# Performance work log

Measured on AMD Instinct MI355X. Metric: run time of the kernel, lower is better.

## Reference

```python
import jax, jax.numpy as jnp
import numpy as np
from jax import lax

B, IMG = 2, 512
FMC, HID, A, NC = 1024, 512, 9, 21
RED, POOL, TOP, IOU_THR = 16, 7, 20, 0.3
NEG = -1e30
# 3 scales x 3 aspect ratios (w, h)
ANCHOR_WH = np.array([[s * np.sqrt(r), s / np.sqrt(r)] for s in (64.0, 128.0, 256.0) for r in (0.5, 1.0, 2.0)], dtype=np.float32)


def conv(x, w, b, stride, pad):
    y = lax.conv_general_dilated(x, w, (stride, stride), pad, dimension_numbers=('NCHW', 'OIHW', 'NCHW'))
    return y + b[None, :, None, None]


def make_anchors(H, W, stride):
    cy = (jnp.arange(H, dtype=jnp.float32) + 0.5) * stride
    cx = (jnp.arange(W, dtype=jnp.float32) + 0.5) * stride
    cyg, cxg = jnp.meshgrid(cy, cx, indexing='ij')  # [H,W]
    wh = jnp.asarray(ANCHOR_WH)  # [A,2]
    w2 = wh[None, None, :, 0] / 2
    h2 = wh[None, None, :, 1] / 2
    cxg = cxg[:, :, None]
    cyg = cyg[:, :, None]
    boxes = jnp.stack([cxg - w2, cyg - h2, cxg + w2, cyg + h2], axis=-1)  # [H,W,A,4]
    return boxes.reshape(-1, 4)


def box_iou(b, boxes):
    # b [4], boxes [N,4], (x1,y1,x2,y2)
    ix1 = jnp.maximum(b[0], boxes[:, 0])
    iy1 = jnp.maximum(b[1], boxes[:, 1])
    ix2 = jnp.minimum(b[2], boxes[:, 2])
    iy2 = jnp.minimum(b[3], boxes[:, 3])
    inter = jnp.maximum(ix2 - ix1, 0.0) * jnp.maximum(iy2 - iy1, 0.0)
    ab = jnp.maximum(b[2] - b[0], 0.0) * jnp.maximum(b[3] - b[1], 0.0)
    ar = jnp.maximum(boxes[:, 2] - boxes[:, 0], 0.0) * jnp.maximum(boxes[:, 3] - boxes[:, 1], 0.0)
    return inter / (ab + ar - inter + 1e-8)


def nms_one(boxes, scores):
    # greedy NMS, fixed TOP selections
    n = scores.shape[0]
    idxs = jnp.arange(n)

    def step(s, _):
        i = jnp.argmax(s)
        b, sc = boxes[i], s[i]
        s = jnp.where((box_iou(b, boxes) > IOU_THR) | (idxs == i), NEG, s)
        return s, (b, sc)

    _, (bs, ss) = lax.scan(step, scores, None, length=TOP)
    return bs, ss  # [TOP,4], [TOP]


def roi_align_one(fm_b, boxes):
    # fm_b [C,H,W], boxes [R,4] in image coords -> [R,C,POOL,POOL]
    C, H, W = fm_b.shape
    b = boxes / RED
    t = (jnp.arange(POOL, dtype=jnp.float32) + 0.5) / POOL
    xs = b[:, 0:1] + jnp.maximum(b[:, 2] - b[:, 0], 0.0)[:, None] * t[None]  # [R,P]
    ys = b[:, 1:2] + jnp.maximum(b[:, 3] - b[:, 1], 0.0)[:, None] * t[None]
    x = jnp.clip(xs[:, None, :], 0.0, W - 1.0) * jnp.ones((1, POOL, 1), jnp.float32)  # [R,P,P]
    y = jnp.clip(ys[:, :, None], 0.0, H - 1.0) * jnp.ones((1, 1, POOL), jnp.float32)
    x0f, y0f = jnp.floor(x), jnp.floor(y)
    x0, y0 = x0f.astype(jnp.int32), y0f.astype(jnp.int32)
    x1 = jnp.minimum(x0 + 1, W - 1)
    y1 = jnp.minimum(y0 + 1, H - 1)
    lx, ly = x - x0f, y - y0f
    v00 = fm_b[:, y0, x0]
    v01 = fm_b[:, y0, x1]
    v10 = fm_b[:, y1, x0]
    v11 = fm_b[:, y1, x1]  # [C,R,P,P]
    out = v00 * (1 - ly) * (1 - lx) + v01 * (1 - ly) * lx + v10 * ly * (1 - lx) + v11 * ly * lx
    return out.transpose(1, 0, 2, 3)


def setup_inputs() -> dict:
    key = jax.random.key(0)
    ks = jax.random.split(key, 16)
    s = 0.02
    return {
        'img': jax.random.normal(ks[0], (B, 3, IMG, IMG), jnp.float32),
        'img_id': jnp.arange(B, dtype=jnp.int32),
        'cnn_w': jax.random.normal(ks[1], (FMC, 3, RED, RED), jnp.float32) * s,
        'cnn_b': jnp.zeros((FMC,), jnp.float32),
        'rpn_w': jax.random.normal(ks[2], (HID, FMC, 3, 3), jnp.float32) * s,
        'rpn_b': jnp.zeros((HID,), jnp.float32),
        'rpn_reg_w': jax.random.normal(ks[3], (A * 4, HID, 1, 1), jnp.float32) * s,
        'rpn_reg_b': jnp.zeros((A * 4,), jnp.float32),
        'rpn_cls_w': jax.random.normal(ks[4], (A, HID, 1, 1), jnp.float32) * s,
        'rpn_cls_b': jnp.zeros((A,), jnp.float32),
        'fc_w': jax.random.normal(ks[5], (FMC * POOL * POOL, 1024), jnp.float32) * 0.005,
        'fc_b': jnp.zeros((1024,), jnp.float32),
        'reg_w': jax.random.normal(ks[6], (1024, 4), jnp.float32) * s,
        'reg_b': jnp.zeros((4,), jnp.float32),
        'cls_w': jax.random.normal(ks[7], (1024, NC), jnp.float32) * s,
        'cls_b': jnp.zeros((NC,), jnp.float32),
    }


def reference(img, img_id, cnn_w, cnn_b, rpn_w, rpn_b, rpn_reg_w, rpn_reg_b, rpn_cls_w, rpn_cls_b, fc_w, fc_b, reg_w, reg_b, cls_w, cls_b):
    fm = jax.nn.relu(conv(img, cnn_w, cnn_b, RED, 'VALID'))  # [B,1024,32,32]
    Bn, C, H, W = fm.shape
    # sliding-window(3x3, stride 1) + per-slice RPN == 3x3 SAME conv + 1x1 heads
    h = jax.nn.relu(conv(fm, rpn_w, rpn_b, 1, 'SAME'))
    rpn_reg = conv(h, rpn_reg_w, rpn_reg_b, 1, 'SAME').transpose(0, 2, 3, 1).reshape(Bn, -1, 4)  # (h,w,a) order
    rpn_cls = conv(h, rpn_cls_w, rpn_cls_b, 1, 'SAME').transpose(0, 2, 3, 1).reshape(Bn, -1)
    anchors = make_anchors(H, W, RED)  # [H*W*A,4]
    nms_reg, nms_cls = jax.vmap(nms_one)(rpn_reg + anchors[None], rpn_cls)  # [B,TOP,4],[B,TOP]
    pooled = jax.vmap(roi_align_one)(fm[img_id], nms_reg)  # [B,TOP,C,P,P]
    flat = pooled.reshape(Bn * TOP, -1)
    hf = jax.nn.relu(flat @ fc_w + fc_b)
    rcnn_reg = (hf @ reg_w + reg_b).reshape(Bn, -1, 4)
    rcnn_cls = (hf @ cls_w + cls_b).reshape(Bn, TOP, -1)
    return rpn_reg, rpn_cls, nms_reg, nms_cls, rcnn_reg, rcnn_cls, anchors
```

## Files before the change

### kernel.cpp

```cpp
#include <hip/hip_runtime.h>
#include <math.h>


#define NEGV (-1e30f)

typedef unsigned short u16;
typedef float v4f __attribute__((ext_vector_type(4)));
typedef short short8 __attribute__((ext_vector_type(8)));

#define O_RPN_REG 0
#define O_RPN_CLS 73728
#define O_NMS_REG 92160
#define O_NMS_CLS 92320
#define O_RCNN_REG 92360
#define O_RCNN_CLS 92520
#define O_ANCH 93360

#define W_FM   0u
#define W_ZERO 2097152u
#define W_PROP 3145728u
#define W_SCR  3219456u
#define W_FLAT 3237888u
#define W_HF   5244928u
#define W_A1H  5285888u
#define W_A1L  6072320u
#define W_B1H  6858752u
#define W_B1L  7251968u
#define W_FMH  7645184u
#define W_FML  8693760u
#define W_B2H  9742336u
#define W_B2L  12101632u
#define W_PART 14460928u

static __device__ __forceinline__ float relu_(float v) { return fmaxf(v, 0.0f); }

static __device__ __forceinline__ void gload16(const void* g, void* l) {
    __builtin_amdgcn_global_load_lds(
        (const __attribute__((address_space(1))) unsigned int*)g,
        (__attribute__((address_space(3))) unsigned int*)l, 16, 0, 0);
}

static __device__ __forceinline__ u16 bf16_rtne(float x) {
    unsigned int u = __float_as_uint(x);
    unsigned int r = u + 0x7fffu + ((u >> 16) & 1u);
    return (u16)(r >> 16);
}
static __device__ __forceinline__ void split2(float x, u16& h, u16& l) {
    h = bf16_rtne(x);
    const float hf = __uint_as_float(((unsigned int)h) << 16);
    l = bf16_rtne(x - hf);
}
static __device__ __forceinline__ void split8_store(const float* v, u16* dsth, u16* dstl) {
    uint4 H, Lo;
    u16 h0, l0, h1, l1;
    split2(v[0], h0, l0); split2(v[1], h1, l1);
    H.x = (unsigned)h0 | ((unsigned)h1 << 16); Lo.x = (unsigned)l0 | ((unsigned)l1 << 16);
    split2(v[2], h0, l0); split2(v[3], h1, l1);
    H.y = (unsigned)h0 | ((unsigned)h1 << 16); Lo.y = (unsigned)l0 | ((unsigned)l1 << 16);
    split2(v[4], h0, l0); split2(v[5], h1, l1);
    H.z = (unsigned)h0 | ((unsigned)h1 << 16); Lo.z = (unsigned)l0 | ((unsigned)l1 << 16);
    split2(v[6], h0, l0); split2(v[7], h1, l1);
    H.w = (unsigned)h0 | ((unsigned)h1 << 16); Lo.w = (unsigned)l0 | ((unsigned)l1 << 16);
    *(uint4*)dsth = H; *(uint4*)dstl = Lo;
}

static __device__ __forceinline__ void anchor_wh(int a, float& w2, float& h2) {
    double s = (a < 3) ? 64.0 : (a < 6) ? 128.0 : 256.0;
    int rm = a - (a / 3) * 3;
    double r = (rm == 0) ? 0.5 : (rm == 1) ? 1.0 : 2.0;
    double sq = sqrt(r);
    w2 = (float)(s * sq) * 0.5f;
    h2 = (float)(s / sq) * 0.5f;
}

__global__ __launch_bounds__(256) void k_prep_all(
        const float* __restrict__ img, u16* __restrict__ a1h, u16* __restrict__ a1l,
        float* __restrict__ zbuf,
        const float* __restrict__ cnnw, u16* __restrict__ b1h, u16* __restrict__ b1l,
        const float* __restrict__ rpnw, u16* __restrict__ b2h, u16* __restrict__ b2l) {
    __shared__ __align__(16) u16 sh[9216];
    __shared__ __align__(16) u16 sl[9216];
    const int bx = blockIdx.x, tid = threadIdx.x;
    if (bx < 1536) {
        if (bx == 0 && tid < 64) zbuf[tid] = 0.0f;
        const int idx = bx * 256 + tid;
        const int m = idx / 192, kq = (idx - m * 192) * 4;
        const int b = m >> 10, i = (m >> 5) & 31, j = m & 31;
        const int c = kq >> 8, rem = kq & 255, y = rem >> 4, x = rem & 15;
        const float4 v = *(const float4*)(img + ((size_t)((b * 3 + c) * 512 + i * 16 + y)) * 512 + j * 16 + x);
        ushort4 H, Lo;
        split2(v.x, H.x, Lo.x); split2(v.y, H.y, Lo.y);
        split2(v.z, H.z, Lo.z); split2(v.w, H.w, Lo.w);
        *(ushort4*)(a1h + (size_t)idx * 4) = H;
        *(ushort4*)(a1l + (size_t)idx * 4) = Lo;
    } else if (bx < 2304) {
        const int idx = (bx - 1536) * 256 + tid;
        const float4 v = *(const float4*)(cnnw + (size_t)idx * 4);
        ushort4 H, Lo;
        split2(v.x, H.x, Lo.x); split2(v.y, H.y, Lo.y);
        split2(v.z, H.z, Lo.z); split2(v.w, H.w, Lo.w);
        *(ushort4*)(b1h + (size_t)idx * 4) = H;
        *(ushort4*)(b1l + (size_t)idx * 4) = Lo;
    } else {
        const int oc = bx - 2304;
        const float* p = rpnw + (size_t)oc * 9216;
        for (int i = tid * 4; i < 9216; i += 1024) {
            const float4 v = *(const float4*)(p + i);
            ushort4 H, Lo;
            split2(v.x, H.x, Lo.x); split2(v.y, H.y, Lo.y);
            split2(v.z, H.z, Lo.z); split2(v.w, H.w, Lo.w);
            *(ushort4*)(sh + i) = H;
            *(ushort4*)(sl + i) = Lo;
        }
        __syncthreads();
        const int ic4 = tid * 4;
#pragma unroll
        for (int d = 0; d < 9; ++d) {
            ushort4 H, Lo;
            H.x = sh[(ic4 + 0) * 9 + d]; Lo.x = sl[(ic4 + 0) * 9 + d];
            H.y = sh[(ic4 + 1) * 9 + d]; Lo.y = sl[(ic4 + 1) * 9 + d];
            H.z = sh[(ic4 + 2) * 9 + d]; Lo.z = sl[(ic4 + 2) * 9 + d];
            H.w = sh[(ic4 + 3) * 9 + d]; Lo.w = sl[(ic4 + 3) * 9 + d];
            const size_t o = (size_t)oc * 9216 + d * 1024 + ic4;
            *(ushort4*)(b2h + o) = H;
            *(ushort4*)(b2l + o) = Lo;
        }
    }
}

template<int MODE>
__global__ __launch_bounds__(256, 3) void k_gemm(
        const u16* __restrict__ Agh, const u16* __restrict__ Agl,
        const u16* __restrict__ Bgh, const u16* __restrict__ Bgl,
        const float* __restrict__ bias, float* __restrict__ Cout, float* __restrict__ Cout2,
        const int KA, const int KB, const int nchunk, const int ldc, const int do_bias_relu,
        u16* __restrict__ outH, u16* __restrict__ outL, const float* __restrict__ zbuf) {
    __shared__ __align__(16) u16 AsH[2 * 128 * 32];
    __shared__ __align__(16) u16 AsL[2 * 128 * 32];
    __shared__ __align__(16) u16 BsH[2 * 64 * 32];
    __shared__ __align__(16) u16 BsL[2 * 64 * 32];
    const int tid = threadIdx.x;
    const int w = tid >> 6, L = tid & 63;
    const int q = L >> 4, lr = L & 15;
    const int wm = w >> 1, wn = w & 1;
    const int m0 = blockIdx.x * 128, n0 = blockIdx.y * 64;
    const int zbase = blockIdx.z * nchunk;
    float* C;
    if (MODE == 1) {
        C = (blockIdx.z < 4) ? (Cout + (size_t)blockIdx.z * (2048u * 512u))
                             : (Cout2 + (size_t)(blockIdx.z - 4) * (2048u * 512u));
    } else {
        C = (blockIdx.z == 0) ? Cout : Cout2;
    }
    const int seg = L & 3, rsub = L >> 2;

    u16* lseg[6];
    int lsz[6];
    const u16* gbase[6];
    int arow_b[6], arow_i[6], arow_j[6];
    int kindv[6];
#pragma unroll
    for (int s = 0; s < 6; ++s) {
        const int idx = w * 6 + s;
        int kind, inst;
        if (idx < 8)       { kind = 0; inst = idx; }
        else if (idx < 16) { kind = 1; inst = idx - 8; }
        else if (idx < 20) { kind = 2; inst = idx - 16; }
        else               { kind = 3; inst = idx - 20; }
        kindv[s] = kind;
        const int r = inst * 16 + rsub;
        u16* lb = (kind == 0) ? AsH : (kind == 1) ? AsL : (kind == 2) ? BsH : BsL;
        lseg[s] = lb + r * 32 + seg * 8;
        lsz[s] = (kind < 2) ? (128 * 32) : (64 * 32);
        arow_b[s] = 0; arow_i[s] = 0; arow_j[s] = 0;
        if (kind >= 2) {
            const u16* gb = (kind == 2) ? Bgh : Bgl;
            gbase[s] = gb + (size_t)(n0 + r) * KB + seg * 8;
        } else if (MODE == 0) {
            const u16* gb = (kind == 0) ? Agh : Agl;
            gbase[s] = gb + (size_t)(m0 + r) * KA + seg * 8;
        } else {
            const int m = m0 + r;
            arow_b[s] = m >> 10; arow_i[s] = (m >> 5) & 31; arow_j[s] = m & 31;
            gbase[s] = (kind == 0) ? Agh : Agl;
        }
    }

    v4f acc[4][2];
#pragma unroll
    for (int t = 0; t < 4; ++t)
#pragma unroll
        for (int u2 = 0; u2 < 2; ++u2) acc[t][u2] = (v4f){0.f, 0.f, 0.f, 0.f};

#define ISSUE(c_, bb_) do { \
    int d_, ic_, kB_; \
    if (MODE == 0) { const int g_ = zbase + (c_); kB_ = g_ * 32; d_ = 0; ic_ = kB_; } \
    else { const int g_ = zbase + (c_); d_ = g_ >> 5; ic_ = (g_ & 31) << 5; kB_ = d_ * 1024 + ic_; } \
    const int di_ = d_ / 3, dj_ = d_ - di_ * 3; \
    _Pragma("unroll") \
    for (int s = 0; s < 6; ++s) { \
        const u16* gsrc_; \
        if (kindv[s] >= 2) gsrc_ = gbase[s] + kB_; \
        else if (MODE == 0) gsrc_ = gbase[s] + ic_; \
        else { \
            const int y_ = arow_i[s] + di_ - 1, x_ = arow_j[s] + dj_ - 1; \
            const bool ok_ = ((unsigned)y_ < 32u) && ((unsigned)x_ < 32u); \
            const int yc_ = ok_ ? y_ : 0, xc_ = ok_ ? x_ : 0; \
            const u16* ga_ = gbase[s] + (size_t)((arow_b[s] * 32 + yc_) * 32 + xc_) * 1024 + ic_ + seg * 8; \
            gsrc_ = ok_ ? ga_ : (const u16*)zbuf; \
        } \
        gload16(gsrc_, lseg[s] + (bb_) * lsz[s]); \
    } \
} while (0)

    int cur = 0;
    ISSUE(0, 0);
    for (int c = 0; c < nchunk; ++c) {
        __syncthreads();
        if (c + 1 < nchunk) ISSUE(c + 1, cur ^ 1);
        const int ao = cur * (128 * 32), bo = cur * (64 * 32);
        short8 ah[4], al[4], bh[2], bl[2];
#pragma unroll
        for (int t = 0; t < 4; ++t) {
            ah[t] = *(const short8*)(AsH + ao + (wm * 64 + t * 16 + lr) * 32 + q * 8);
            al[t] = *(const short8*)(AsL + ao + (wm * 64 + t * 16 + lr) * 32 + q * 8);
        }
#pragma unroll
        for (int u2 = 0; u2 < 2; ++u2) {
            bh[u2] = *(const short8*)(BsH + bo + (wn * 32 + u2 * 16 + lr) * 32 + q * 8);
            bl[u2] = *(const short8*)(BsL + bo + (wn * 32 + u2 * 16 + lr) * 32 + q * 8);
        }
#pragma unroll
        for (int t = 0; t < 4; ++t)
#pragma unroll
            for (int u2 = 0; u2 < 2; ++u2) {
                acc[t][u2] = __builtin_amdgcn_mfma_f32_16x16x32_bf16(ah[t], bh[u2], acc[t][u2], 0, 0, 0);
                acc[t][u2] = __builtin_amdgcn_mfma_f32_16x16x32_bf16(ah[t], bl[u2], acc[t][u2], 0, 0, 0);
                acc[t][u2] = __builtin_amdgcn_mfma_f32_16x16x32_bf16(al[t], bh[u2], acc[t][u2], 0, 0, 0);
            }
        cur ^= 1;
    }
#undef ISSUE

#pragma unroll
    for (int t = 0; t < 4; ++t) {
        const int row = m0 + wm * 64 + t * 16 + q * 4;
#pragma unroll
        for (int u2 = 0; u2 < 2; ++u2) {
            const int col = n0 + wn * 32 + u2 * 16 + lr;
            const float bv = do_bias_relu ? bias[col] : 0.f;
#pragma unroll
            for (int r = 0; r < 4; ++r) {
                float vv = acc[t][u2][r];
                if (do_bias_relu) vv = relu_(vv + bv);
                C[(size_t)(row + r) * ldc + col] = vv;
                if (MODE == 0 && outH != nullptr) {
                    u16 hh, ll; split2(vv, hh, ll);
                    outH[(size_t)(row + r) * 1024 + col] = hh;
                    outL[(size_t)(row + r) * 1024 + col] = ll;
                }
            }
        }
    }
}

__global__ void k_c1_reduce(const float* __restrict__ p1, const float* __restrict__ cb,
                            float* __restrict__ fm, u16* __restrict__ fmh, u16* __restrict__ fml) {
    const size_t o = ((size_t)blockIdx.x * 256 + threadIdx.x) * 4;
    float4 a = *(const float4*)(fm + o);
    const float4 b4 = *(const float4*)(p1 + o);
    const float4 bb = *(const float4*)(cb + (o & 1023));
    a.x = relu_(a.x + b4.x + bb.x);
    a.y = relu_(a.y + b4.y + bb.y);
    a.z = relu_(a.z + b4.z + bb.z);
    a.w = relu_(a.w + b4.w + bb.w);
    *(float4*)(fm + o) = a;
    ushort4 H, Lo;
    split2(a.x, H.x, Lo.x); split2(a.y, H.y, Lo.y);
    split2(a.z, H.z, Lo.z); split2(a.w, H.w, Lo.w);
    *(ushort4*)(fmh + o) = H;
    *(ushort4*)(fml + o) = Lo;
}

__global__ __launch_bounds__(256) void k_rpn_heads2(const float* __restrict__ partA,
        const float* __restrict__ partB,
        const float* __restrict__ rpnb,
        const float* __restrict__ regw, const float* __restrict__ regb,
        const float* __restrict__ clsw, const float* __restrict__ clsb,
        float* __restrict__ out, float* __restrict__ prop, float* __restrict__ scr) {
    __shared__ __align__(16) float hrow[8][512];
    const int tid = threadIdx.x;
    const int m0 = blockIdx.x * 8;
#pragma unroll
    for (int i = 0; i < 4; ++i) {
        const int f = i * 256 + tid;
        const int r = f >> 7, c4 = (f & 127) * 4;
        const size_t ro = (size_t)(m0 + r) * 512 + c4;
        const float4 a0 = *(const float4*)(partA + ro);
        const float4 a1 = *(const float4*)(partA + 1048576u + ro);
        const float4 a2 = *(const float4*)(partA + 2097152u + ro);
        const float4 a3 = *(const float4*)(partA + 3145728u + ro);
        const float4 a4 = *(const float4*)(partB + ro);
        const float4 a5 = *(const float4*)(partB + 1048576u + ro);
        const float4 bb = *(const float4*)(rpnb + c4);
        float4 o;
        o.x = relu_(a0.x + a1.x + a2.x + a3.x + a4.x + a5.x + bb.x);
        o.y = relu_(a0.y + a1.y + a2.y + a3.y + a4.y + a5.y + bb.y);
        o.z = relu_(a0.z + a1.z + a2.z + a3.z + a4.z + a5.z + bb.z);
        o.w = relu_(a0.w + a1.w + a2.w + a3.w + a4.w + a5.w + bb.w);
        *(float4*)&hrow[r][c4] = o;
    }
    __syncthreads();
    const int w = tid >> 6, lane = tid & 63;
#pragma unroll
    for (int rr = 0; rr < 2; ++rr) {
        const int lrow = w * 2 + rr;
        const int m = m0 + lrow;
        const int b = m >> 10, qd = m & 1023, ii = qd >> 5, jj = qd & 31;
        const float cx = ((float)jj + 0.5f) * 16.f, cy = ((float)ii + 0.5f) * 16.f;
        if (lane < 45) {
            const int isreg = (lane < 36);
            const float* wp = isreg ? (regw + (size_t)lane * 512) : (clsw + (size_t)(lane - 36) * 512);
            float acc2 = isreg ? regb[lane] : clsb[lane - 36];
            const float* hr = hrow[lrow];
            for (int k = 0; k < 512; k += 4) {
                const float4 wv = *(const float4*)(wp + k);
                acc2 += hr[k + 0] * wv.x; acc2 += hr[k + 1] * wv.y;
                acc2 += hr[k + 2] * wv.z; acc2 += hr[k + 3] * wv.w;
            }
            if (isreg) {
                out[O_RPN_REG + (size_t)b * 36864 + qd * 36 + lane] = acc2;
                const int a = lane >> 2, cc = lane & 3;
                float w2, h2; anchor_wh(a, w2, h2);
                const float av = (cc == 0) ? cx - w2 : (cc == 1) ? cy - h2 : (cc == 2) ? cx + w2 : cy + h2;
                prop[(size_t)b * 36864 + qd * 36 + lane] = acc2 + av;
            } else {
                const int n = lane - 36;
                out[O_RPN_CLS + (size_t)b * 9216 + qd * 9 + n] = acc2;
                scr[(size_t)b * 9216 + qd * 9 + n] = acc2;
            }
        } else if (b == 0 && lane < 54) {
            const int a = lane - 45;
            float w2, h2; anchor_wh(a, w2, h2);
            const float4 av4 = make_float4(cx - w2, cy - h2, cx + w2, cy + h2);
            *(float4*)(out + O_ANCH + (size_t)(qd * 9 + a) * 4) = av4;
        }
    }
}

__global__ __launch_bounds__(512) void k_nms3(const float* __restrict__ prop,
        const float* __restrict__ scr, float* __restrict__ out) {
    __shared__ float wv_[2][8];
    __shared__ int wi_[2][8];
    const int b = blockIdx.x, tid = threadIdx.x;
    const int lane = tid & 63, wid = tid >> 6;
    const float* P = prop + (size_t)b * 36864;
    float4 bx[18]; float sv[18];
#pragma unroll
    for (int k = 0; k < 18; ++k) {
        const int i = tid * 18 + k;
        bx[k] = *(const float4*)(P + (size_t)i * 4);
        sv[k] = scr[b * 9216 + i];
    }
    for (int t = 0; t < 20; ++t) {
        float bv = -3.4e38f; int bi = 0;
#pragma unroll
        for (int k = 0; k < 18; ++k)
            if (sv[k] > bv) { bv = sv[k]; bi = tid * 18 + k; }
#pragma unroll
        for (int off = 1; off < 64; off <<= 1) {
            const float ov = __shfl_xor(bv, off);
            const int oi = __shfl_xor(bi, off);
            if (ov > bv || (ov == bv && oi < bi)) { bv = ov; bi = oi; }
        }
        if (lane == 0) { wv_[t & 1][wid] = bv; wi_[t & 1][wid] = bi; }
        __syncthreads();
        float rb = wv_[t & 1][0]; int sel = wi_[t & 1][0];
#pragma unroll
        for (int j = 1; j < 8; ++j) {
            const float v2 = wv_[t & 1][j]; const int i2 = wi_[t & 1][j];
            if (v2 > rb || (v2 == rb && i2 < sel)) { rb = v2; sel = i2; }
        }
        const float4 bb = *(const float4*)(P + (size_t)sel * 4);
        if (tid == 0) {
            *(float4*)(out + O_NMS_REG + (size_t)(b * 20 + t) * 4) = bb;
            out[O_NMS_CLS + b * 20 + t] = rb;
        }
        const float ab2 = fmaxf(bb.z - bb.x, 0.f) * fmaxf(bb.w - bb.y, 0.f);
#pragma unroll
        for (int k = 0; k < 18; ++k) {
            const float ix1 = fmaxf(bb.x, bx[k].x), iy1 = fmaxf(bb.y, bx[k].y);
            const float ix2 = fminf(bb.z, bx[k].z), iy2 = fminf(bb.w, bx[k].w);
            const float inter = fmaxf(ix2 - ix1, 0.f) * fmaxf(iy2 - iy1, 0.f);
            const float ar2 = fmaxf(bx[k].z - bx[k].x, 0.f) * fmaxf(bx[k].w - bx[k].y, 0.f);
            const float iou = inter / (ab2 + ar2 - inter + 1e-8f);
            if (iou > 0.3f || (tid * 18 + k) == sel) sv[k] = NEGV;
        }
    }
}

__global__ __launch_bounds__(256) void k_roi(const float* __restrict__ fm,
        const int* __restrict__ img_id, const float* __restrict__ nreg,
        float* __restrict__ flat, const float* __restrict__ fcb, float* __restrict__ hf) {
    __shared__ float tile[12544];
    const int hid = (((blockIdx.z * 20 + blockIdx.y) * 4) + blockIdx.x) * 256 + threadIdx.x;
    hf[hid] = fcb[hid & 1023];
    const int c0 = blockIdx.x * 256;
    const int roi = blockIdx.y, b = blockIdx.z;
    const float* bx = nreg + (size_t)(b * 20 + roi) * 4;
    const float b0 = bx[0] * 0.0625f, b1 = bx[1] * 0.0625f;
    const float b2 = bx[2] * 0.0625f, b3 = bx[3] * 0.0625f;
    const float wd = fmaxf(b2 - b0, 0.f), hg = fmaxf(b3 - b1, 0.f);
    const int bb = img_id[b];
    const float* fmb = fm + (size_t)bb * (32 * 32 * 1024);
    const int c = c0 + threadIdx.x;
    for (int py = 0; py < 7; ++py) {
        const float tyv = ((float)py + 0.5f) / 7.0f;
        const float ycv = fminf(fmaxf(b1 + hg * tyv, 0.f), 31.f);
        const float y0f = floorf(ycv);
        const int y0 = (int)y0f, y1 = min(y0 + 1, 31);
        const float ly = ycv - y0f, omly = 1.f - ly;
        for (int px = 0; px < 7; ++px) {
            const float txv = ((float)px + 0.5f) / 7.0f;
            const float xcv = fminf(fmaxf(b0 + wd * txv, 0.f), 31.f);
            const float x0f = floorf(xcv);
            const int x0 = (int)x0f, x1 = min(x0 + 1, 31);
            const float lx = xcv - x0f, omlx = 1.f - lx;
            const int o00 = ((y0 * 32) + x0) << 10, o01 = ((y0 * 32) + x1) << 10;
            const int o10 = ((y1 * 32) + x0) << 10, o11 = ((y1 * 32) + x1) << 10;
            const float v00 = fmb[o00 + c], v01 = fmb[o01 + c];
            const float v10 = fmb[o10 + c], v11 = fmb[o11 + c];
            tile[threadIdx.x * 49 + py * 7 + px] =
                ((v00 * omly) * omlx) + ((v01 * omly) * lx)
                + ((v10 * ly) * omlx) + ((v11 * ly) * lx);
        }
    }
    __syncthreads();
    const size_t ob = (size_t)(b * 20 + roi) * 50176 + (size_t)c0 * 49;
    for (int i = threadIdx.x * 4; i < 12544; i += 1024)
        *(float4*)(flat + ob + i) = *(const float4*)&tile[i];
}

__global__ __launch_bounds__(256, 2) void k_fc_mfma(const float* __restrict__ flat,
        const float* __restrict__ fcw, float* __restrict__ hf) {
    __shared__ __align__(16) u16 AsH[4 * 48 * 8];
    __shared__ __align__(16) u16 AsL[4 * 48 * 8];
    __shared__ __align__(16) u16 BsH[4 * 128 * 8];
    __shared__ __align__(16) u16 BsL[4 * 128 * 8];
    const int tid = threadIdx.x;
    const int w = tid >> 6, L = tid & 63, q = L >> 4, lr = L & 15;
    const int n0 = blockIdx.x * 128, kb = blockIdx.y * 512;
    if (tid < 32) {
        const int oct = tid >> 3, m = 40 + (tid & 7);
        *(uint4*)(AsH + (oct * 48 + m) * 8) = make_uint4(0, 0, 0, 0);
        *(uint4*)(AsL + (oct * 48 + m) * 8) = make_uint4(0, 0, 0, 0);
    }
    const int am = tid >> 2, aoct = tid & 3;
    const float* abase = flat + (size_t)am * 50176 + kb + aoct * 8;
    const int bcolI = tid & 127, bkh = tid >> 7;
    const float* bcol = fcw + n0 + bcolI;

    v4f acc[3][2];
#pragma unroll
    for (int mt = 0; mt < 3; ++mt)
#pragma unroll
        for (int nt = 0; nt < 2; ++nt) acc[mt][nt] = (v4f){0.f, 0.f, 0.f, 0.f};

    float areg[8];
    float breg[2][8];

#define LOADF(c_) do { \
    if (tid < 160) { \
        const float4 u_ = *(const float4*)(abase + (c_) * 32); \
        const float4 v_ = *(const float4*)(abase + (c_) * 32 + 4); \
        areg[0] = u_.x; areg[1] = u_.y; areg[2] = u_.z; areg[3] = u_.w; \
        areg[4] = v_.x; areg[5] = v_.y; areg[6] = v_.z; areg[7] = v_.w; \
    } \
    _Pragma("unroll") \
    for (int o_ = 0; o_ < 2; ++o_) \
        _Pragma("unroll") \
        for (int j_ = 0; j_ < 8; ++j_) \
            breg[o_][j_] = bcol[(size_t)(kb + (c_) * 32 + bkh * 16 + o_ * 8 + j_) * 1024]; \
} while (0)

    LOADF(0);
    for (int c = 0; c < 16; ++c) {
        __syncthreads();
        if (tid < 160)
            split8_store(areg, AsH + (aoct * 48 + am) * 8, AsL + (aoct * 48 + am) * 8);
#pragma unroll
        for (int o = 0; o < 2; ++o)
            split8_store(breg[o], BsH + ((bkh * 2 + o) * 128 + bcolI) * 8,
                                  BsL + ((bkh * 2 + o) * 128 + bcolI) * 8);
        __syncthreads();
        if (c + 1 < 16) LOADF(c + 1);
        short8 ah[3], al[3], bh2[2], bl2[2];
#pragma unroll
        for (int mt = 0; mt < 3; ++mt) {
            ah[mt] = *(const short8*)(AsH + (q * 48 + mt * 16 + lr) * 8);
            al[mt] = *(const short8*)(AsL + (q * 48 + mt * 16 + lr) * 8);
        }
#pragma unroll
        for (int nt = 0; nt < 2; ++nt) {
            bh2[nt] = *(const short8*)(BsH + (q * 128 + w * 32 + nt * 16 + lr) * 8);
            bl2[nt] = *(const short8*)(BsL + (q * 128 + w * 32 + nt * 16 + lr) * 8);
        }
#pragma unroll
        for (int mt = 0; mt < 3; ++mt)
#pragma unroll
            for (int nt = 0; nt < 2; ++nt) {
                acc[mt][nt] = __builtin_amdgcn_mfma_f32_16x16x32_bf16(ah[mt], bh2[nt], acc[mt][nt], 0, 0, 0);
                acc[mt][nt] = __builtin_amdgcn_mfma_f32_16x16x32_bf16(ah[mt], bl2[nt], acc[mt][nt], 0, 0, 0);
                acc[mt][nt] = __builtin_amdgcn_mfma_f32_16x16x32_bf16(al[mt], bh2[nt], acc[mt][nt], 0, 0, 0);
            }
    }
#undef LOADF

#pragma unroll
    for (int mt = 0; mt < 3; ++mt) {
#pragma unroll
        for (int nt = 0; nt < 2; ++nt) {
#pragma unroll
            for (int r = 0; r < 4; ++r) {
                const int row = mt * 16 + q * 4 + r;
                if (row < 40)
                    atomicAdd(hf + (size_t)row * 1024 + n0 + w * 32 + nt * 16 + lr, acc[mt][nt][r]);
            }
        }
    }
}

__global__ __launch_bounds__(64) void k_heads(const float* __restrict__ hf,
        const float* __restrict__ regw, const float* __restrict__ regb,
        const float* __restrict__ clsw, const float* __restrict__ clsb,
        float* __restrict__ out) {
    __shared__ __align__(16) float hrow[1024];
    const int m = blockIdx.x, tid = threadIdx.x;
    for (int i = tid * 4; i < 1024; i += 256) {
        const float4 v = *(const float4*)(hf + (size_t)m * 1024 + i);
        hrow[i + 0] = relu_(v.x); hrow[i + 1] = relu_(v.y);
        hrow[i + 2] = relu_(v.z); hrow[i + 3] = relu_(v.w);
    }
    __syncthreads();
    if (tid < 25) {
        float acc2 = 0.f;
        if (tid < 4) {
            for (int k = 0; k < 1024; ++k) acc2 += hrow[k] * regw[(size_t)k * 4 + tid];
            out[O_RCNN_REG + m * 4 + tid] = acc2 + regb[tid];
        } else {
            const int n = tid - 4;
            for (int k = 0; k < 1024; ++k) acc2 += hrow[k] * clsw[(size_t)k * 21 + n];
            out[O_RCNN_CLS + m * 21 + n] = acc2 + clsb[n];
        }
    }
}

extern "C" void kernel_launch(void* const* d_in, const int* in_sizes, int n_in,
                              void* d_out, int out_size, void* d_ws, size_t ws_size,
                              hipStream_t stream) {
    (void)in_sizes; (void)n_in; (void)out_size; (void)ws_size;
    const float* img       = (const float*)d_in[0];
    const int*   img_id    = (const int*)  d_in[1];
    const float* cnn_w     = (const float*)d_in[2];
    const float* cnn_b     = (const float*)d_in[3];
    const float* rpn_w     = (const float*)d_in[4];
    const float* rpn_b     = (const float*)d_in[5];
    const float* rpn_reg_w = (const float*)d_in[6];
    const float* rpn_reg_b = (const float*)d_in[7];
    const float* rpn_cls_w = (const float*)d_in[8];
    const float* rpn_cls_b = (const float*)d_in[9];
    const float* fc_w      = (const float*)d_in[10];
    const float* fc_b      = (const float*)d_in[11];
    const float* reg_w     = (const float*)d_in[12];
    const float* reg_b     = (const float*)d_in[13];
    const float* cls_w     = (const float*)d_in[14];
    const float* cls_b     = (const float*)d_in[15];
    float* out = (float*)d_out;
    float* ws  = (float*)d_ws;

    float* fm   = ws + W_FM;
    float* zbuf = ws + W_ZERO;
    float* prop = ws + W_PROP;
    float* scr  = ws + W_SCR;
    float* flat = ws + W_FLAT;
    float* hf   = ws + W_HF;
    u16* a1h = (u16*)(ws + W_A1H);
    u16* a1l = (u16*)(ws + W_A1L);
    u16* b1h = (u16*)(ws + W_B1H);
    u16* b1l = (u16*)(ws + W_B1L);
    u16* fmh = (u16*)(ws + W_FMH);
    u16* fml = (u16*)(ws + W_FML);
    u16* b2h = (u16*)(ws + W_B2H);
    u16* b2l = (u16*)(ws + W_B2L);
    float* partA = ws + W_FLAT;
    float* partB = ws + W_PART;

    k_prep_all<<<2816, 256, 0, stream>>>(img, a1h, a1l, zbuf, cnn_w, b1h, b1l, rpn_w, b2h, b2l);
    k_gemm<0><<<dim3(16, 16, 2), 256, 0, stream>>>(a1h, a1l, b1h, b1l, cnn_b, fm, partB,
                                                   768, 768, 12, 1024, 0, nullptr, nullptr, zbuf);
    k_c1_reduce<<<2048, 256, 0, stream>>>(partB, cnn_b, fm, fmh, fml);
    k_gemm<1><<<dim3(16, 8, 6), 256, 0, stream>>>(fmh, fml, b2h, b2l, nullptr, partA, partB,
                                                  1024, 9216, 48, 512, 0, nullptr, nullptr, zbuf);
    k_rpn_heads2<<<256, 256, 0, stream>>>(partA, partB, rpn_b, rpn_reg_w, rpn_reg_b, rpn_cls_w, rpn_cls_b,
                                          out, prop, scr);
    k_nms3<<<2, 512, 0, stream>>>(prop, scr, out);
    k_roi<<<dim3(4, 20, 2), 256, 0, stream>>>(fm, img_id, out + O_NMS_REG, flat, fc_b, hf);
    k_fc_mfma<<<dim3(8, 98), 256, 0, stream>>>(flat, fc_w, hf);
    k_heads<<<40, 64, 0, stream>>>(hf, reg_w, reg_b, cls_w, cls_b, out);
}
```

Measured before the change: 605.4 us.

## Interleave hi/lo bf16 splits into swizzled 64-element rows and widen FC tiles

The hi and lo bf16 halves of the GEMM operands are now stored interleaved in one buffer, 32 hi then 32 lo per k-chunk. This lets each GEMM stage load both halves with one contiguous 128-byte global-to-LDS copy into a single XOR-swizzled LDS tile, replacing separate hi/lo buffers and loads. The aim is fewer load instructions, better coalescing and fewer LDS bank conflicts. The prep kernel is split into three launches, which adds launch overhead, and the FC kernel tile is widened from 128 to 256 columns so half as many blocks each do more MFMA work per loaded A tile.

```diff
diff --git a/kernel.cpp b/kernel.cpp
--- a/kernel.cpp
+++ b/kernel.cpp
@@ -22,14 +22,10 @@
 #define W_SCR  3219456u
 #define W_FLAT 3237888u
 #define W_HF   5244928u
-#define W_A1H  5285888u
-#define W_A1L  6072320u
-#define W_B1H  6858752u
-#define W_B1L  7251968u
-#define W_FMH  7645184u
-#define W_FML  8693760u
-#define W_B2H  9742336u
-#define W_B2L  12101632u
+#define W_A1I  5285888u
+#define W_B1I  6858752u
+#define W_FMI  7645184u
+#define W_B2I  9742336u
 #define W_PART 14460928u
 
 static __device__ __forceinline__ float relu_(float v) { return fmaxf(v, 0.0f); }
@@ -73,72 +69,72 @@
     h2 = (float)(s / sq) * 0.5f;
 }
 
-__global__ __launch_bounds__(256) void k_prep_all(
-        const float* __restrict__ img, u16* __restrict__ a1h, u16* __restrict__ a1l,
-        float* __restrict__ zbuf,
-        const float* __restrict__ cnnw, u16* __restrict__ b1h, u16* __restrict__ b1l,
-        const float* __restrict__ rpnw, u16* __restrict__ b2h, u16* __restrict__ b2l) {
+
+__global__ void k_prep_a1(const float* __restrict__ img, u16* __restrict__ a1i,
+                          float* __restrict__ zbuf) {
+    if (blockIdx.x == 0 && threadIdx.x < 64) zbuf[threadIdx.x] = 0.0f;
+    const int idx = blockIdx.x * 256 + threadIdx.x;
+    const int m = idx / 192, k = (idx - m * 192) * 4;
+    const int b = m >> 10, i = (m >> 5) & 31, j = m & 31;
+    const int c = k >> 8, rem = k & 255, y = rem >> 4, x = rem & 15;
+    const float4 v = *(const float4*)(img + ((size_t)((b * 3 + c) * 512 + i * 16 + y)) * 512 + j * 16 + x);
+    ushort4 H, Lo;
+    split2(v.x, H.x, Lo.x); split2(v.y, H.y, Lo.y);
+    split2(v.z, H.z, Lo.z); split2(v.w, H.w, Lo.w);
+    const size_t base = ((size_t)m * 24 + (k >> 5)) * 64 + (k & 31);
+    *(ushort4*)(a1i + base) = H;
+    *(ushort4*)(a1i + base + 32) = Lo;
+}
+
+__global__ void k_prep_b1(const float* __restrict__ src, u16* __restrict__ b1i) {
+    const int idx = blockIdx.x * 256 + threadIdx.x;
+    const int p = idx * 4;
+    const int n = p / 768, k = p - n * 768;
+    const float4 v = *(const float4*)(src + (size_t)p);
+    ushort4 H, Lo;
+    split2(v.x, H.x, Lo.x); split2(v.y, H.y, Lo.y);
+    split2(v.z, H.z, Lo.z); split2(v.w, H.w, Lo.w);
+    const size_t base = ((size_t)n * 24 + (k >> 5)) * 64 + (k & 31);
+    *(ushort4*)(b1i + base) = H;
+    *(ushort4*)(b1i + base + 32) = Lo;
+}
+
+__global__ __launch_bounds__(256) void k_prep_w2(const float* __restrict__ w,
+        u16* __restrict__ b2i) {
     __shared__ __align__(16) u16 sh[9216];
     __shared__ __align__(16) u16 sl[9216];
-    const int bx = blockIdx.x, tid = threadIdx.x;
-    if (bx < 1536) {
-        if (bx == 0 && tid < 64) zbuf[tid] = 0.0f;
-        const int idx = bx * 256 + tid;
-        const int m = idx / 192, kq = (idx - m * 192) * 4;
-        const int b = m >> 10, i = (m >> 5) & 31, j = m & 31;
-        const int c = kq >> 8, rem = kq & 255, y = rem >> 4, x = rem & 15;
-        const float4 v = *(const float4*)(img + ((size_t)((b * 3 + c) * 512 + i * 16 + y)) * 512 + j * 16 + x);
+    const int oc = blockIdx.x;
+    const float* p = w + (size_t)oc * 9216;
+    for (int i = threadIdx.x * 4; i < 9216; i += 1024) {
+        const float4 v = *(const float4*)(p + i);
         ushort4 H, Lo;
         split2(v.x, H.x, Lo.x); split2(v.y, H.y, Lo.y);
         split2(v.z, H.z, Lo.z); split2(v.w, H.w, Lo.w);
-        *(ushort4*)(a1h + (size_t)idx * 4) = H;
-        *(ushort4*)(a1l + (size_t)idx * 4) = Lo;
-    } else if (bx < 2304) {
-        const int idx = (bx - 1536) * 256 + tid;
-        const float4 v = *(const float4*)(cnnw + (size_t)idx * 4);
+        *(ushort4*)(sh + i) = H;
+        *(ushort4*)(sl + i) = Lo;
+    }
+    __syncthreads();
+    const int ic4 = threadIdx.x * 4;
+#pragma unroll
+    for (int d = 0; d < 9; ++d) {
         ushort4 H, Lo;
-        split2(v.x, H.x, Lo.x); split2(v.y, H.y, Lo.y);
-        split2(v.z, H.z, Lo.z); split2(v.w, H.w, Lo.w);
-        *(ushort4*)(b1h + (size_t)idx * 4) = H;
-        *(ushort4*)(b1l + (size_t)idx * 4) = Lo;
-    } else {
-        const int oc = bx - 2304;
-        const float* p = rpnw + (size_t)oc * 9216;
-        for (int i = tid * 4; i < 9216; i += 1024) {
-            const float4 v = *(const float4*)(p + i);
-            ushort4 H, Lo;
-            split2(v.x, H.x, Lo.x); split2(v.y, H.y, Lo.y);
-            split2(v.z, H.z, Lo.z); split2(v.w, H.w, Lo.w);
-            *(ushort4*)(sh + i) = H;
-            *(ushort4*)(sl + i) = Lo;
-        }
-        __syncthreads();
-        const int ic4 = tid * 4;
-#pragma unroll
-        for (int d = 0; d < 9; ++d) {
-            ushort4 H, Lo;
-            H.x = sh[(ic4 + 0) * 9 + d]; Lo.x = sl[(ic4 + 0) * 9 + d];
-            H.y = sh[(ic4 + 1) * 9 + d]; Lo.y = sl[(ic4 + 1) * 9 + d];
-            H.z = sh[(ic4 + 2) * 9 + d]; Lo.z = sl[(ic4 + 2) * 9 + d];
-            H.w = sh[(ic4 + 3) * 9 + d]; Lo.w = sl[(ic4 + 3) * 9 + d];
-            const size_t o = (size_t)oc * 9216 + d * 1024 + ic4;
-            *(ushort4*)(b2h + o) = H;
-            *(ushort4*)(b2l + o) = Lo;
-        }
+        H.x = sh[(ic4 + 0) * 9 + d]; Lo.x = sl[(ic4 + 0) * 9 + d];
+        H.y = sh[(ic4 + 1) * 9 + d]; Lo.y = sl[(ic4 + 1) * 9 + d];
+        H.z = sh[(ic4 + 2) * 9 + d]; Lo.z = sl[(ic4 + 2) * 9 + d];
+        H.w = sh[(ic4 + 3) * 9 + d]; Lo.w = sl[(ic4 + 3) * 9 + d];
+        const size_t base = ((size_t)oc * 288 + d * 32 + (ic4 >> 5)) * 64 + (ic4 & 31);
+        *(ushort4*)(b2i + base) = H;
+        *(ushort4*)(b2i + base + 32) = Lo;
     }
 }
 
 template<int MODE>
 __global__ __launch_bounds__(256, 3) void k_gemm(
-        const u16* __restrict__ Agh, const u16* __restrict__ Agl,
-        const u16* __restrict__ Bgh, const u16* __restrict__ Bgl,
-        const float* __restrict__ bias, float* __restrict__ Cout, float* __restrict__ Cout2,
-        const int KA, const int KB, const int nchunk, const int ldc, const int do_bias_relu,
-        u16* __restrict__ outH, u16* __restrict__ outL, const float* __restrict__ zbuf) {
-    __shared__ __align__(16) u16 AsH[2 * 128 * 32];
-    __shared__ __align__(16) u16 AsL[2 * 128 * 32];
-    __shared__ __align__(16) u16 BsH[2 * 64 * 32];
-    __shared__ __align__(16) u16 BsL[2 * 64 * 32];
+        const u16* __restrict__ Agi, const u16* __restrict__ Bgi,
+        float* __restrict__ Cout, float* __restrict__ Cout2,
+        const int AstrU, const int BstrU, const int nchunk, const int ldc,
+        const float* __restrict__ zbuf) {
+    __shared__ __align__(16) u16 Ls[2 * 192 * 64];
     const int tid = threadIdx.x;
     const int w = tid >> 6, L = tid & 63;
     const int q = L >> 4, lr = L & 15;
@@ -152,39 +148,28 @@
     } else {
         C = (blockIdx.z == 0) ? Cout : Cout2;
     }
-    const int seg = L & 3, rsub = L >> 2;
-
-    u16* lseg[6];
-    int lsz[6];
+    const int rr8 = tid >> 3;
+    const int segp = (tid & 7) ^ (rr8 & 7);
+
     const u16* gbase[6];
-    int arow_b[6], arow_i[6], arow_j[6];
-    int kindv[6];
+    int mi[4], mj[4];
 #pragma unroll
     for (int s = 0; s < 6; ++s) {
-        const int idx = w * 6 + s;
-        int kind, inst;
-        if (idx < 8)       { kind = 0; inst = idx; }
-        else if (idx < 16) { kind = 1; inst = idx - 8; }
-        else if (idx < 20) { kind = 2; inst = idx - 16; }
-        else               { kind = 3; inst = idx - 20; }
-        kindv[s] = kind;
-        const int r = inst * 16 + rsub;
-        u16* lb = (kind == 0) ? AsH : (kind == 1) ? AsL : (kind == 2) ? BsH : BsL;
-        lseg[s] = lb + r * 32 + seg * 8;
-        lsz[s] = (kind < 2) ? (128 * 32) : (64 * 32);
-        arow_b[s] = 0; arow_i[s] = 0; arow_j[s] = 0;
-        if (kind >= 2) {
-            const u16* gb = (kind == 2) ? Bgh : Bgl;
-            gbase[s] = gb + (size_t)(n0 + r) * KB + seg * 8;
+        if (s >= 4) {
+            const int br = n0 + (s - 4) * 32 + rr8;
+            gbase[s] = Bgi + (size_t)br * BstrU + segp * 8;
         } else if (MODE == 0) {
-            const u16* gb = (kind == 0) ? Agh : Agl;
-            gbase[s] = gb + (size_t)(m0 + r) * KA + seg * 8;
+            gbase[s] = Agi + (size_t)(m0 + s * 32 + rr8) * AstrU + segp * 8;
         } else {
-            const int m = m0 + r;
-            arow_b[s] = m >> 10; arow_i[s] = (m >> 5) & 31; arow_j[s] = m & 31;
-            gbase[s] = (kind == 0) ? Agh : Agl;
-        }
-    }
+            const int m = m0 + s * 32 + rr8;
+            const int b_ = m >> 10;
+            mi[s] = (m >> 5) & 31; mj[s] = m & 31;
+            gbase[s] = Agi + (size_t)b_ * 2097152 + segp * 8;
+        }
+    }
+    const int x7 = lr & 7;
+    const int shh = (q ^ x7) << 3;
+    const int shl = ((4 + q) ^ x7) << 3;
 
     v4f acc[4][2];
 #pragma unroll
@@ -193,23 +178,21 @@
         for (int u2 = 0; u2 < 2; ++u2) acc[t][u2] = (v4f){0.f, 0.f, 0.f, 0.f};
 
 #define ISSUE(c_, bb_) do { \
-    int d_, ic_, kB_; \
-    if (MODE == 0) { const int g_ = zbase + (c_); kB_ = g_ * 32; d_ = 0; ic_ = kB_; } \
-    else { const int g_ = zbase + (c_); d_ = g_ >> 5; ic_ = (g_ & 31) << 5; kB_ = d_ * 1024 + ic_; } \
+    const int g_ = zbase + (c_); \
+    int d_ = 0, icc_ = 0; \
+    if (MODE == 1) { d_ = g_ >> 5; icc_ = g_ & 31; } \
     const int di_ = d_ / 3, dj_ = d_ - di_ * 3; \
     _Pragma("unroll") \
     for (int s = 0; s < 6; ++s) { \
         const u16* gsrc_; \
-        if (kindv[s] >= 2) gsrc_ = gbase[s] + kB_; \
-        else if (MODE == 0) gsrc_ = gbase[s] + ic_; \
+        if (s >= 4 || MODE == 0) gsrc_ = gbase[s] + (size_t)g_ * 64; \
         else { \
-            const int y_ = arow_i[s] + di_ - 1, x_ = arow_j[s] + dj_ - 1; \
+            const int y_ = mi[s] + di_ - 1, x_ = mj[s] + dj_ - 1; \
             const bool ok_ = ((unsigned)y_ < 32u) && ((unsigned)x_ < 32u); \
-            const int yc_ = ok_ ? y_ : 0, xc_ = ok_ ? x_ : 0; \
-            const u16* ga_ = gbase[s] + (size_t)((arow_b[s] * 32 + yc_) * 32 + xc_) * 1024 + ic_ + seg * 8; \
-            gsrc_ = ok_ ? ga_ : (const u16*)zbuf; \
+            gsrc_ = ok_ ? (gbase[s] + (size_t)(((y_ * 32) + x_) * 32 + icc_) * 64) \
+                        : ((const u16*)zbuf + segp * 8); \
         } \
-        gload16(gsrc_, lseg[s] + (bb_) * lsz[s]); \
+        gload16(gsrc_, Ls + (bb_) * 12288 + s * 2048 + tid * 8); \
     } \
 } while (0)
 
@@ -218,17 +201,19 @@
     for (int c = 0; c < nchunk; ++c) {
         __syncthreads();
         if (c + 1 < nchunk) ISSUE(c + 1, cur ^ 1);
-        const int ao = cur * (128 * 32), bo = cur * (64 * 32);
+        const int ao = cur * 12288;
         short8 ah[4], al[4], bh[2], bl[2];
 #pragma unroll
         for (int t = 0; t < 4; ++t) {
-            ah[t] = *(const short8*)(AsH + ao + (wm * 64 + t * 16 + lr) * 32 + q * 8);
-            al[t] = *(const short8*)(AsL + ao + (wm * 64 + t * 16 + lr) * 32 + q * 8);
+            const int rowA = wm * 64 + t * 16 + lr;
+            ah[t] = *(const short8*)(Ls + ao + rowA * 64 + shh);
+            al[t] = *(const short8*)(Ls + ao + rowA * 64 + shl);
         }
 #pragma unroll
         for (int u2 = 0; u2 < 2; ++u2) {
-            bh[u2] = *(const short8*)(BsH + bo + (wn * 32 + u2 * 16 + lr) * 32 + q * 8);
-            bl[u2] = *(const short8*)(BsL + bo + (wn * 32 + u2 * 16 + lr) * 32 + q * 8);
+            const int rowB = 128 + wn * 32 + u2 * 16 + lr;
+            bh[u2] = *(const short8*)(Ls + ao + rowB * 64 + shh);
+            bl[u2] = *(const short8*)(Ls + ao + rowB * 64 + shl);
         }
 #pragma unroll
         for (int t = 0; t < 4; ++t)
@@ -248,25 +233,17 @@
 #pragma unroll
         for (int u2 = 0; u2 < 2; ++u2) {
             const int col = n0 + wn * 32 + u2 * 16 + lr;
-            const float bv = do_bias_relu ? bias[col] : 0.f;
-#pragma unroll
-            for (int r = 0; r < 4; ++r) {
-                float vv = acc[t][u2][r];
-                if (do_bias_relu) vv = relu_(vv + bv);
-                C[(size_t)(row + r) * ldc + col] = vv;
-                if (MODE == 0 && outH != nullptr) {
-                    u16 hh, ll; split2(vv, hh, ll);
-                    outH[(size_t)(row + r) * 1024 + col] = hh;
-                    outL[(size_t)(row + r) * 1024 + col] = ll;
-                }
-            }
+#pragma unroll
+            for (int r = 0; r < 4; ++r)
+                C[(size_t)(row + r) * ldc + col] = acc[t][u2][r];
         }
     }
 }
 
 __global__ void k_c1_reduce(const float* __restrict__ p1, const float* __restrict__ cb,
-                            float* __restrict__ fm, u16* __restrict__ fmh, u16* __restrict__ fml) {
-    const size_t o = ((size_t)blockIdx.x * 256 + threadIdx.x) * 4;
+                            float* __restrict__ fm, u16* __restrict__ fmi) {
+    const int gid = blockIdx.x * 256 + threadIdx.x;
+    const size_t o = (size_t)gid * 4;
     float4 a = *(const float4*)(fm + o);
     const float4 b4 = *(const float4*)(p1 + o);
     const float4 bb = *(const float4*)(cb + (o & 1023));
@@ -278,8 +255,10 @@
     ushort4 H, Lo;
     split2(a.x, H.x, Lo.x); split2(a.y, H.y, Lo.y);
     split2(a.z, H.z, Lo.z); split2(a.w, H.w, Lo.w);
-    *(ushort4*)(fmh + o) = H;
-    *(ushort4*)(fml + o) = Lo;
+    const int m = (int)(o >> 10), ic = (int)(o & 1023);
+    const size_t base = ((size_t)m * 32 + (ic >> 5)) * 64 + (ic & 31);
+    *(ushort4*)(fmi + base) = H;
+    *(ushort4*)(fmi + base + 32) = Lo;
 }
 
 __global__ __launch_bounds__(256) void k_rpn_heads2(const float* __restrict__ partA,
@@ -445,11 +424,11 @@
         const float* __restrict__ fcw, float* __restrict__ hf) {
     __shared__ __align__(16) u16 AsH[4 * 48 * 8];
     __shared__ __align__(16) u16 AsL[4 * 48 * 8];
-    __shared__ __align__(16) u16 BsH[4 * 128 * 8];
-    __shared__ __align__(16) u16 BsL[4 * 128 * 8];
+    __shared__ __align__(16) u16 BsH[4 * 256 * 8];
+    __shared__ __align__(16) u16 BsL[4 * 256 * 8];
     const int tid = threadIdx.x;
     const int w = tid >> 6, L = tid & 63, q = L >> 4, lr = L & 15;
-    const int n0 = blockIdx.x * 128, kb = blockIdx.y * 512;
+    const int n0 = blockIdx.x * 256, kb = blockIdx.y * 512;
     if (tid < 32) {
         const int oct = tid >> 3, m = 40 + (tid & 7);
         *(uint4*)(AsH + (oct * 48 + m) * 8) = make_uint4(0, 0, 0, 0);
@@ -457,17 +436,16 @@
     }
     const int am = tid >> 2, aoct = tid & 3;
     const float* abase = flat + (size_t)am * 50176 + kb + aoct * 8;
-    const int bcolI = tid & 127, bkh = tid >> 7;
-    const float* bcol = fcw + n0 + bcolI;
-
-    v4f acc[3][2];
+    const float* bcol = fcw + n0 + tid;
+
+    v4f acc[3][4];
 #pragma unroll
     for (int mt = 0; mt < 3; ++mt)
 #pragma unroll
-        for (int nt = 0; nt < 2; ++nt) acc[mt][nt] = (v4f){0.f, 0.f, 0.f, 0.f};
+        for (int nt = 0; nt < 4; ++nt) acc[mt][nt] = (v4f){0.f, 0.f, 0.f, 0.f};
 
     float areg[8];
-    float breg[2][8];
+    float breg[4][8];
 
 #define LOADF(c_) do { \
     if (tid < 160) { \
@@ -477,10 +455,10 @@
         areg[4] = v_.x; areg[5] = v_.y; areg[6] = v_.z; areg[7] = v_.w; \
     } \
     _Pragma("unroll") \
-    for (int o_ = 0; o_ < 2; ++o_) \
+    for (int o_ = 0; o_ < 4; ++o_) \
         _Pragma("unroll") \
         for (int j_ = 0; j_ < 8; ++j_) \
-            breg[o_][j_] = bcol[(size_t)(kb + (c_) * 32 + bkh * 16 + o_ * 8 + j_) * 1024]; \
+            breg[o_][j_] = bcol[(size_t)(kb + (c_) * 32 + o_ * 8 + j_) * 1024]; \
 } while (0)
 
     LOADF(0);
@@ -489,26 +467,25 @@
         if (tid < 160)
             split8_store(areg, AsH + (aoct * 48 + am) * 8, AsL + (aoct * 48 + am) * 8);
 #pragma unroll
-        for (int o = 0; o < 2; ++o)
-            split8_store(breg[o], BsH + ((bkh * 2 + o) * 128 + bcolI) * 8,
-                                  BsL + ((bkh * 2 + o) * 128 + bcolI) * 8);
+        for (int o = 0; o < 4; ++o)
+            split8_store(breg[o], BsH + (o * 256 + tid) * 8, BsL + (o * 256 + tid) * 8);
         __syncthreads();
         if (c + 1 < 16) LOADF(c + 1);
-        short8 ah[3], al[3], bh2[2], bl2[2];
+        short8 ah[3], al[3], bh2[4], bl2[4];
 #pragma unroll
         for (int mt = 0; mt < 3; ++mt) {
             ah[mt] = *(const short8*)(AsH + (q * 48 + mt * 16 + lr) * 8);
             al[mt] = *(const short8*)(AsL + (q * 48 + mt * 16 + lr) * 8);
         }
 #pragma unroll
-        for (int nt = 0; nt < 2; ++nt) {
-            bh2[nt] = *(const short8*)(BsH + (q * 128 + w * 32 + nt * 16 + lr) * 8);
-            bl2[nt] = *(const short8*)(BsL + (q * 128 + w * 32 + nt * 16 + lr) * 8);
+        for (int nt = 0; nt < 4; ++nt) {
+            bh2[nt] = *(const short8*)(BsH + (q * 256 + w * 64 + nt * 16 + lr) * 8);
+            bl2[nt] = *(const short8*)(BsL + (q * 256 + w * 64 + nt * 16 + lr) * 8);
         }
 #pragma unroll
         for (int mt = 0; mt < 3; ++mt)
 #pragma unroll
-            for (int nt = 0; nt < 2; ++nt) {
+            for (int nt = 0; nt < 4; ++nt) {
                 acc[mt][nt] = __builtin_amdgcn_mfma_f32_16x16x32_bf16(ah[mt], bh2[nt], acc[mt][nt], 0, 0, 0);
                 acc[mt][nt] = __builtin_amdgcn_mfma_f32_16x16x32_bf16(ah[mt], bl2[nt], acc[mt][nt], 0, 0, 0);
                 acc[mt][nt] = __builtin_amdgcn_mfma_f32_16x16x32_bf16(al[mt], bh2[nt], acc[mt][nt], 0, 0, 0);
@@ -519,12 +496,12 @@
 #pragma unroll
     for (int mt = 0; mt < 3; ++mt) {
 #pragma unroll
-        for (int nt = 0; nt < 2; ++nt) {
+        for (int nt = 0; nt < 4; ++nt) {
 #pragma unroll
             for (int r = 0; r < 4; ++r) {
                 const int row = mt * 16 + q * 4 + r;
                 if (row < 40)
-                    atomicAdd(hf + (size_t)row * 1024 + n0 + w * 32 + nt * 16 + lr, acc[mt][nt][r]);
+                    atomicAdd(hf + (size_t)row * 1024 + n0 + w * 64 + nt * 16 + lr, acc[mt][nt][r]);
             }
         }
     }
@@ -584,27 +561,25 @@
     float* scr  = ws + W_SCR;
     float* flat = ws + W_FLAT;
     float* hf   = ws + W_HF;
-    u16* a1h = (u16*)(ws + W_A1H);
-    u16* a1l = (u16*)(ws + W_A1L);
-    u16* b1h = (u16*)(ws + W_B1H);
-    u16* b1l = (u16*)(ws + W_B1L);
-    u16* fmh = (u16*)(ws + W_FMH);
-    u16* fml = (u16*)(ws + W_FML);
-    u16* b2h = (u16*)(ws + W_B2H);
-    u16* b2l = (u16*)(ws + W_B2L);
+    u16* a1i = (u16*)(ws + W_A1I);
+    u16* b1i = (u16*)(ws + W_B1I);
+    u16* fmi = (u16*)(ws + W_FMI);
+    u16* b2i = (u16*)(ws + W_B2I);
     float* partA = ws + W_FLAT;
     float* partB = ws + W_PART;
 
-    k_prep_all<<<2816, 256, 0, stream>>>(img, a1h, a1l, zbuf, cnn_w, b1h, b1l, rpn_w, b2h, b2l);
-    k_gemm<0><<<dim3(16, 16, 2), 256, 0, stream>>>(a1h, a1l, b1h, b1l, cnn_b, fm, partB,
-                                                   768, 768, 12, 1024, 0, nullptr, nullptr, zbuf);
-    k_c1_reduce<<<2048, 256, 0, stream>>>(partB, cnn_b, fm, fmh, fml);
-    k_gemm<1><<<dim3(16, 8, 6), 256, 0, stream>>>(fmh, fml, b2h, b2l, nullptr, partA, partB,
-                                                  1024, 9216, 48, 512, 0, nullptr, nullptr, zbuf);
-    k_rpn_heads2<<<256, 256, 0, stream>>>(partA, partB, rpn_b, rpn_reg_w, rpn_reg_b, rpn_cls_w, rpn_cls_b,
-                                          out, prop, scr);
+    k_prep_a1<<<1536, 256, 0, stream>>>(img, a1i, zbuf);
+    k_prep_b1<<<768, 256, 0, stream>>>(cnn_w, b1i);
+    k_prep_w2<<<512, 256, 0, stream>>>(rpn_w, b2i);
+    k_gemm<0><<<dim3(16, 16, 2), 256, 0, stream>>>(a1i, b1i, fm, partB,
+                                                   24 * 64, 24 * 64, 12, 1024, zbuf);
+    k_c1_reduce<<<2048, 256, 0, stream>>>(partB, cnn_b, fm, fmi);
+    k_gemm<1><<<dim3(16, 8, 6), 256, 0, stream>>>(fmi, b2i, partA, partB,
+                                                  0, 288 * 64, 48, 512, zbuf);
+    k_rpn_heads2<<<256, 256, 0, stream>>>(partA, partB, rpn_b, rpn_reg_w, rpn_reg_b,
+                                          rpn_cls_w, rpn_cls_b, out, prop, scr);
     k_nms3<<<2, 512, 0, stream>>>(prop, scr, out);
     k_roi<<<dim3(4, 20, 2), 256, 0, stream>>>(fm, img_id, out + O_NMS_REG, flat, fc_b, hf);
-    k_fc_mfma<<<dim3(8, 98), 256, 0, stream>>>(flat, fc_w, hf);
+    k_fc_mfma<<<dim3(4, 98), 256, 0, stream>>>(flat, fc_w, hf);
     k_heads<<<40, 64, 0, stream>>>(hf, reg_w, reg_b, cls_w, cls_b, out);
 }
```

Result: faster. 581.8 us (-3.9%).
